# Kernel optimization log

Measured on AMD Instinct MI355X. Metric: run time of the kernel, lower is better.

## Reference

```python
import jax, jax.numpy as jnp
import numpy as np

B, S, H, K, HOP = 32, 512, 768, 4, 3


def setup_inputs() -> dict:
    key = jax.random.key(0)
    ks = jax.random.split(key, 18)
    sc = 0.02
    n = lambda k, shp: (jax.random.normal(k, shp, dtype=jnp.float32) * sc)
    inp = {
        "question": jax.random.normal(ks[0], (B, H), dtype=jnp.float32),
        "text": jax.random.normal(ks[1], (B, S, H), dtype=jnp.float32),
        # per-head MultiheadAttention params (stored as [in,out], i.e. W.T of torch Linear)
        "pw_W": n(ks[2], (K, H, H)), "pw_b": n(ks[3], (K, H)),
        "Ws_W": n(ks[4], (K, H, H)), "Ws_b": n(ks[5], (K, H)),
        "Wt_W": n(ks[6], (K, H, H)), "Wt_b": n(ks[7], (K, H)),
        "We_W": n(ks[8], (K, H)), "We_b": n(ks[9], (K,)),
        # head_weight: Linear(K -> 1)
        "headw_W": n(ks[10], (K,)), "headw_b": n(ks[11], (1,)),
        # GRUCell(input=2H, hidden=H); stored as [in, 3H] (r,z,n order as torch)
        "gru_Wih": n(ks[12], (2 * H, 3 * H)), "gru_Whh": n(ks[13], (H, 3 * H)),
        "gru_bih": n(ks[14], (3 * H,)), "gru_bhh": n(ks[15], (3 * H,)),
        "is_training": 0,
    }
    return inp


def _gru_cell(x, h, Wih, Whh, bih, bhh):
    gx = x @ Wih + bih            # [B,3H]
    gh = h @ Whh + bhh            # [B,3H]
    xr, xz, xn = jnp.split(gx, 3, axis=-1)
    hr, hz, hn = jnp.split(gh, 3, axis=-1)
    r = jax.nn.sigmoid(xr + hr)
    z = jax.nn.sigmoid(xz + hz)
    n = jnp.tanh(xn + r * hn)
    return (1.0 - z) * n + z * h


def reference(question, text, pw_W, pw_b, Ws_W, Ws_b, Wt_W, Wt_b, We_W, We_b,
              headw_W, headw_b, gru_Wih, gru_Whh, gru_bih, gru_bhh, is_training):
    # Dropout layers act as identity (eval mode).
    batch_idx = jnp.arange(text.shape[0])
    # text projection + W_s(text) are question-independent -> hoist out of hop loop
    text_p = jnp.einsum('bsh,khj->kbsj', text, pw_W) + pw_b[:, None, None, :]   # [K,B,S,H]
    W_hs = jnp.einsum('kbsh,khj->kbsj', text_p, Ws_W) + Ws_b[:, None, None, :]  # [K,B,S,H]

    h = jnp.zeros((text.shape[0], H), dtype=question.dtype)
    h_states = []
    predict_prob = None
    for hop in range(HOP):
        W_ht = jnp.einsum('bh,khj->kbj', question, Wt_W) + Wt_b[:, None, :]     # [K,B,H]
        scores = jnp.einsum('kbsh,kh->kbs', jnp.tanh(W_hs + W_ht[:, :, None, :]), We_W) \
                 + We_b[:, None, None]                                          # [K,B,S]
        alpha = jax.nn.softmax(scores, axis=2)                                  # softmax over S
        alpha_linear = jnp.einsum('kbs,k->bs', alpha, headw_W) + headw_b        # [B,S]
        scale = jnp.sqrt(jnp.sum(alpha_linear ** 2, axis=1, keepdims=True))
        prob = alpha_linear / scale
        if hop == 0:
            predict_prob = prob
        idx = jnp.argmax(alpha_linear, axis=1)                                  # [B]
        max_text = text[batch_idx, idx]                                         # [B,H]
        x = jnp.concatenate([question, max_text], axis=1)                       # [B,2H]
        h = _gru_cell(x, h, gru_Wih, gru_Whh, gru_bih, gru_bhh)
        h_states.append(h)
        question = h
    return predict_prob, jnp.stack(h_states, axis=1)                            # [B,S],[B,HOP,H]
```

## Files before the change

kernel.cpp:

```cpp
#include <hip/hip_runtime.h>

typedef unsigned short u16;
typedef __bf16 bf16x8 __attribute__((ext_vector_type(8)));
typedef float f32x4 __attribute__((ext_vector_type(4)));

#define NB 32
#define NS 512
#define NH 768
#define NK 4
#define NBS 16384
#define H3 2304
#define HH 589824

__device__ inline float bf2f(u16 u) {
    unsigned x = ((unsigned)u) << 16;
    return __builtin_bit_cast(float, x);
}
__device__ inline u16 f2bf(float f) {
    unsigned u = __builtin_bit_cast(unsigned, f);
    u += 0x7fffu + ((u >> 16) & 1u);
    return (u16)(u >> 16);
}
__device__ inline float tanh_fast(float x) {
    float e = __expf(2.f * x);
    return 1.f - 2.f * __builtin_amdgcn_rcpf(e + 1.f);
}
__device__ inline float sig_fast(float x) {
    return __builtin_amdgcn_rcpf(1.f + __expf(-x));
}
__device__ inline void gld16(const u16* g, u16* l) {
    __builtin_amdgcn_global_load_lds(
        (const __attribute__((address_space(1))) unsigned int*)g,
        (__attribute__((address_space(3))) unsigned int*)l, 16, 0, 0);
}


__global__ void prep_kernel(const float* __restrict__ WsW, const float* __restrict__ pwb,
                            const float* __restrict__ Wsb, float* __restrict__ combB,
                            const float* __restrict__ question,
                            float* __restrict__ q_f32, float* __restrict__ hT,
                            float* __restrict__ sx, float* __restrict__ sh,
                            const float* __restrict__ Web, float* __restrict__ scores,
                            const float* __restrict__ pwW,
                            u16* __restrict__ WsTH, u16* __restrict__ WsTL,
                            u16* __restrict__ pwH, u16* __restrict__ pwL,
                            const float* __restrict__ text, u16* __restrict__ textH,
                            int tier, int splitText)
{
    int bid = blockIdx.x, t = threadIdx.x;
    if (bid < 48) {
        int idx = bid * 64 + (t >> 2);
        int ph = t & 3;
        int k = idx / NH, j = idx % NH;
        const float* W = WsW + (long)k * HH + j;
        const float* pb = pwb + k * NH;
        float acc = 0.f;
        #pragma unroll 8
        for (int m = ph * 192; m < ph * 192 + 192; ++m)
            acc += pb[m] * W[(long)m * NH];
        acc += __shfl_xor(acc, 1);
        acc += __shfl_xor(acc, 2);
        if (ph == 0) combB[idx] = acc + Wsb[idx];
    } else if (bid < 144) {
        int idx = (bid - 48) * 256 + t;
        q_f32[idx] = question[idx];
    } else if (bid < 240) {
        int idx = (bid - 144) * 256 + t;
        hT[idx] = 0.f;
    } else if (bid < 816) {
        int idx = (bid - 240) * 256 + t;
        if (idx < 73728) sx[idx] = 0.f;
        else sh[idx - 73728] = 0.f;
    } else if (bid < 1072) {
        int idx = (bid - 816) * 256 + t;
        scores[idx] = Web[idx >> 14];
    } else if (bid < 3376) {
        if (tier < 2) return;
        __shared__ float tile[32][33];
        int bid2 = bid - 1072;
        int k = bid2 / 576, rem = bid2 % 576, tr = rem / 24, tc = rem % 24;
        const float* src = WsW + (long)k * HH;
        long dbase = (long)k * HH;
        int tx = t & 31, ty = t >> 5;
        #pragma unroll
        for (int i = 0; i < 4; ++i)
            tile[tx][ty + i*8] = src[(long)(tr*32 + ty + i*8) * NH + tc*32 + tx];
        __syncthreads();
        #pragma unroll
        for (int i = 0; i < 4; ++i) {
            float v = tile[ty + i*8][tx];
            u16 hv = f2bf(v);
            u16 lv = f2bf(v - bf2f(hv));
            long o = dbase + (long)(tc*32 + ty + i*8) * NH + tr*32 + tx;
            WsTH[o] = hv; WsTL[o] = lv;
        }
    } else if (bid < 5680) {
        if (tier < 2) return;
        long base = (long)(bid - 3376) * 1024 + t * 4;
        float4 v = *(const float4*)(pwW + base);
        ushort4 hv, lv;
        hv.x = f2bf(v.x); lv.x = f2bf(v.x - bf2f(hv.x));
        hv.y = f2bf(v.y); lv.y = f2bf(v.y - bf2f(hv.y));
        hv.z = f2bf(v.z); lv.z = f2bf(v.z - bf2f(hv.z));
        hv.w = f2bf(v.w); lv.w = f2bf(v.w - bf2f(hv.w));
        *(ushort4*)(pwH + base) = hv;
        *(ushort4*)(pwL + base) = lv;
    } else {
        if (!splitText) return;
        long base = (long)(bid - 5680) * 1024 + t * 4;
        float4 v = *(const float4*)(text + base);
        ushort4 hv;
        hv.x = f2bf(v.x);
        hv.y = f2bf(v.y);
        hv.z = f2bf(v.z);
        hv.w = f2bf(v.w);
        *(ushort4*)(textH + base) = hv;
    }
}

__global__ __launch_bounds__(256) void comb_mfma_kernel(
    const u16* __restrict__ WsTH, const u16* __restrict__ WsTL,
    const u16* __restrict__ pwH, const u16* __restrict__ pwL,
    u16* __restrict__ combTH, u16* __restrict__ combTL)
{
    __shared__ __align__(16) u16 AsH[128 * 32];
    __shared__ __align__(16) u16 AsL[128 * 32];
    __shared__ __align__(16) u16 BsH[128 * 32];
    __shared__ __align__(16) u16 BsL[128 * 32];
    const int t = threadIdx.x;
    const int wave = t >> 6, lane = t & 63;
    const int k = blockIdx.z;
    const long m0 = (long)blockIdx.x * 128;
    const int n0 = blockIdx.y * 128;
    const u16* AH = WsTH + (long)k * HH;
    const u16* AL = WsTL + (long)k * HH;
    const u16* BH = pwH + (long)k * HH;
    const u16* BL = pwL + (long)k * HH;

    const int r = t >> 2, ch = t & 3;
    const int wm = (wave & 1) * 64, wn = (wave >> 1) * 64;
    const int fr = lane & 15, fq = lane >> 4;

    f32x4 acc[4][4];
    #pragma unroll
    for (int i = 0; i < 4; ++i)
        #pragma unroll
        for (int j = 0; j < 4; ++j) acc[i][j] = (f32x4){0.f, 0.f, 0.f, 0.f};

    for (int k0 = 0; k0 < NH; k0 += 32) {
        gld16(AH + (m0 + r)      * NH + k0 + ch*8, AsH + t*8);
        gld16(AH + (m0 + 64 + r) * NH + k0 + ch*8, AsH + 2048 + t*8);
        gld16(AL + (m0 + r)      * NH + k0 + ch*8, AsL + t*8);
        gld16(AL + (m0 + 64 + r) * NH + k0 + ch*8, AsL + 2048 + t*8);
        gld16(BH + (long)(n0 + r)      * NH + k0 + ch*8, BsH + t*8);
        gld16(BH + (long)(n0 + 64 + r) * NH + k0 + ch*8, BsH + 2048 + t*8);
        gld16(BL + (long)(n0 + r)      * NH + k0 + ch*8, BsL + t*8);
        gld16(BL + (long)(n0 + 64 + r) * NH + k0 + ch*8, BsL + 2048 + t*8);
        __syncthreads();
        bf16x8 afH[4], afL[4], bfH[4], bfL[4];
        #pragma unroll
        for (int i = 0; i < 4; ++i) {
            afH[i] = *(const bf16x8*)(AsH + (wm + i*16 + fr)*32 + fq*8);
            afL[i] = *(const bf16x8*)(AsL + (wm + i*16 + fr)*32 + fq*8);
            bfH[i] = *(const bf16x8*)(BsH + (wn + i*16 + fr)*32 + fq*8);
            bfL[i] = *(const bf16x8*)(BsL + (wn + i*16 + fr)*32 + fq*8);
        }
        #pragma unroll
        for (int i = 0; i < 4; ++i)
            #pragma unroll
            for (int j = 0; j < 4; ++j) {
                acc[i][j] = __builtin_amdgcn_mfma_f32_16x16x32_bf16(afH[i], bfH[j], acc[i][j], 0, 0, 0);
                acc[i][j] = __builtin_amdgcn_mfma_f32_16x16x32_bf16(afH[i], bfL[j], acc[i][j], 0, 0, 0);
                acc[i][j] = __builtin_amdgcn_mfma_f32_16x16x32_bf16(afL[i], bfH[j], acc[i][j], 0, 0, 0);
            }
        __syncthreads();
    }
    long kb = (long)k * HH;
    #pragma unroll
    for (int i = 0; i < 4; ++i) {
        long m = m0 + wm + i*16 + fq*4;
        #pragma unroll
        for (int j = 0; j < 4; ++j) {
            long n = n0 + wn + j*16 + fr;
            #pragma unroll
            for (int rr = 0; rr < 4; ++rr) {
                float v = acc[i][j][rr];
                u16 hv = f2bf(v);
                u16 lv = f2bf(v - bf2f(hv));
                combTH[kb + (m + rr) * NH + n] = hv;
                combTL[kb + (m + rr) * NH + n] = lv;
            }
        }
    }
}

__global__ __launch_bounds__(256) void comb_valu_kernel(
    const float* __restrict__ pwW, const float* __restrict__ WsW,
    float* __restrict__ comb)
{
    __shared__ float AtT[32][68];
    __shared__ float Bt[32][132];
    const int t = threadIdx.x;
    const int m0 = blockIdx.x * 64, j0 = blockIdx.y * 128, k = blockIdx.z;
    const float* A = pwW + (long)k * HH;
    const float* B = WsW + (long)k * HH;
    const int r4 = (t >> 4) * 4, c8 = (t & 15) * 8;
    float acc[4][8];
    #pragma unroll
    for (int rr = 0; rr < 4; ++rr)
        #pragma unroll
        for (int cc = 0; cc < 8; ++cc) acc[rr][cc] = 0.f;
    for (int h0 = 0; h0 < NH; h0 += 32) {
        #pragma unroll
        for (int p = 0; p < 8; ++p) {
            int idx = p * 256 + t;
            int r = idx >> 5, hh = idx & 31;
            AtT[hh][r] = A[(long)(m0 + r) * NH + h0 + hh];
        }
        #pragma unroll
        for (int p = 0; p < 16; ++p) {
            int idx = p * 256 + t;
            int hh = idx >> 7, c = idx & 127;
            Bt[hh][c] = B[(long)(h0 + hh) * NH + j0 + c];
        }
        __syncthreads();
        for (int hh = 0; hh < 32; ++hh) {
            float4 av  = *(const float4*)&AtT[hh][r4];
            float4 bv0 = *(const float4*)&Bt[hh][c8];
            float4 bv1 = *(const float4*)&Bt[hh][c8 + 4];
            float a[4] = {av.x, av.y, av.z, av.w};
            float bb[8] = {bv0.x, bv0.y, bv0.z, bv0.w, bv1.x, bv1.y, bv1.z, bv1.w};
            #pragma unroll
            for (int rr = 0; rr < 4; ++rr)
                #pragma unroll
                for (int cc = 0; cc < 8; ++cc) acc[rr][cc] += a[rr] * bb[cc];
        }
        __syncthreads();
    }
    float* C = comb + (long)k * HH;
    #pragma unroll
    for (int rr = 0; rr < 4; ++rr)
        #pragma unroll
        for (int cc = 0; cc < 8; ++cc)
            C[(long)(m0 + r4 + rr) * NH + j0 + c8 + cc] = acc[rr][cc];
}

__global__ void split_combT_kernel(const float* __restrict__ comb,
                                   u16* __restrict__ combTH, u16* __restrict__ combTL)
{
    __shared__ float tile[32][33];
    int bid = blockIdx.x, t = threadIdx.x;
    int k = bid / 576, rem = bid % 576, tr = rem / 24, tc = rem % 24;
    const float* src = comb + (long)k * HH;
    long dbase = (long)k * HH;
    int tx = t & 31, ty = t >> 5;
    #pragma unroll
    for (int i = 0; i < 4; ++i)
        tile[tx][ty + i*8] = src[(long)(tr*32 + ty + i*8) * NH + tc*32 + tx];
    __syncthreads();
    #pragma unroll
    for (int i = 0; i < 4; ++i) {
        float v = tile[ty + i*8][tx];
        u16 hv = f2bf(v);
        u16 lv = f2bf(v - bf2f(hv));
        long o = dbase + (long)(tc*32 + ty + i*8) * NH + tr*32 + tx;
        combTH[o] = hv; combTL[o] = lv;
    }
}

template <int AM>
__global__ __launch_bounds__(256) void tp_gemm_kernel(
    const float* __restrict__ textf, const u16* __restrict__ textH,
    const u16* __restrict__ combTH, const u16* __restrict__ combTL,
    const float* __restrict__ W_ht, const float* __restrict__ WeW,
    u16* __restrict__ TP, float* __restrict__ scores)
{
    __shared__ __align__(16) u16 AsH[128 * 32];
    __shared__ __align__(16) u16 BsH[128 * 32];
    __shared__ __align__(16) u16 BsL[128 * 32];
    __shared__ float wht_s[128];
    __shared__ float we_s[128];
    __shared__ float sred[128];
    const int t = threadIdx.x;
    const int wave = t >> 6, lane = t & 63;
    const int k = blockIdx.z;
    const long m0 = (long)blockIdx.x * 128;
    const int n0 = blockIdx.y * 128;
    const int b = (int)(m0 >> 9), srow = (int)(m0 & 511);
    const u16* BH = combTH + (long)k * HH;
    const u16* BL = combTL + (long)k * HH;

    if (t < 128) {
        wht_s[t] = W_ht[((k << 5) + b) * NH + n0 + t];
        we_s[t]  = WeW[k * NH + n0 + t];
        sred[t]  = 0.f;
    }

    const int r = t >> 2, ch = t & 3;
    const int wm = (wave & 1) * 64, wn = (wave >> 1) * 64;
    const int fr = lane & 15, fq = lane >> 4;

    f32x4 acc[4][4];
    #pragma unroll
    for (int i = 0; i < 4; ++i)
        #pragma unroll
        for (int j = 0; j < 4; ++j) acc[i][j] = (f32x4){0.f, 0.f, 0.f, 0.f};

    for (int h0 = 0; h0 < NH; h0 += 32) {
        if (AM) {
            gld16(textH + (m0 + r)      * NH + h0 + ch*8, AsH + t*8);
            gld16(textH + (m0 + 64 + r) * NH + h0 + ch*8, AsH + 2048 + t*8);
        } else {
            #pragma unroll
            for (int p = 0; p < 4; ++p) {
                int task = p * 256 + t;
                int row = task >> 3, g = task & 7;
                float4 v = *(const float4*)(textf + (m0 + row) * NH + h0 + g*4);
                ushort4 hv;
                hv.x = f2bf(v.x);
                hv.y = f2bf(v.y);
                hv.z = f2bf(v.z);
                hv.w = f2bf(v.w);
                *(ushort4*)(AsH + row * 32 + g*4) = hv;
            }
        }
        gld16(BH + (long)(n0 + r)      * NH + h0 + ch*8, BsH + t*8);
        gld16(BH + (long)(n0 + 64 + r) * NH + h0 + ch*8, BsH + 2048 + t*8);
        gld16(BL + (long)(n0 + r)      * NH + h0 + ch*8, BsL + t*8);
        gld16(BL + (long)(n0 + 64 + r) * NH + h0 + ch*8, BsL + 2048 + t*8);
        __syncthreads();
        bf16x8 afH[4], bfH[4], bfL[4];
        #pragma unroll
        for (int i = 0; i < 4; ++i) {
            afH[i] = *(const bf16x8*)(AsH + (wm + i*16 + fr)*32 + fq*8);
            bfH[i] = *(const bf16x8*)(BsH + (wn + i*16 + fr)*32 + fq*8);
            bfL[i] = *(const bf16x8*)(BsL + (wn + i*16 + fr)*32 + fq*8);
        }
        #pragma unroll
        for (int i = 0; i < 4; ++i)
            #pragma unroll
            for (int j = 0; j < 4; ++j) {
                acc[i][j] = __builtin_amdgcn_mfma_f32_16x16x32_bf16(afH[i], bfH[j], acc[i][j], 0, 0, 0);
                acc[i][j] = __builtin_amdgcn_mfma_f32_16x16x32_bf16(afH[i], bfL[j], acc[i][j], 0, 0, 0);
            }
        __syncthreads();
    }
    u16* out = TP + ((long)k * NBS + m0) * NH + n0;
    #pragma unroll
    for (int i = 0; i < 4; ++i) {
        #pragma unroll
        for (int rr = 0; rr < 4; ++rr) {
            int m = wm + i*16 + fq*4 + rr;
            #pragma unroll
            for (int j = 0; j < 4; ++j) {
                int n = wn + j*16 + fr;
                out[(long)m * NH + n] = f2bf(acc[i][j][rr]);
            }
        }
    }
    #pragma unroll
    for (int i = 0; i < 4; ++i) {
        #pragma unroll
        for (int rr = 0; rr < 4; ++rr) {
            int m = wm + i*16 + fq*4 + rr;
            float part = 0.f;
            #pragma unroll
            for (int j = 0; j < 4; ++j) {
                int n = wn + j*16 + fr;
                part += tanh_fast(acc[i][j][rr] + wht_s[n]) * we_s[n];
            }
            part += __shfl_xor(part, 1);
            part += __shfl_xor(part, 2);
            part += __shfl_xor(part, 4);
            part += __shfl_xor(part, 8);
            if (fr == 0) atomicAdd(&sred[m], part);
        }
    }
    __syncthreads();
    if (t < 128)
        atomicAdd(&scores[(((k << 5) + b) << 9) + srow + t], sred[t]);
}

__global__ __launch_bounds__(256) void score_pass_kernel(
    const u16* __restrict__ TP, const float* __restrict__ W_ht,
    const float* __restrict__ WeW, const float* __restrict__ Web,
    float* __restrict__ scores)
{
    __shared__ __align__(16) float bias_s[NH];
    __shared__ __align__(16) float we_s[NH];
    const int t = threadIdx.x;
    const int k = blockIdx.z, b = blockIdx.y;
    const int s0 = blockIdx.x * 32;
    for (int i = t; i < NH; i += 256) {
        bias_s[i] = W_ht[((k << 5) + b) * NH + i];
        we_s[i]   = WeW[k * NH + i];
    }
    __syncthreads();
    const int wave = t >> 6, lane = t & 63;
    const u16* tpb = TP + ((long)k * NBS + (b << 9) + s0) * NH;
    const float web = Web[k];
    for (int sr = wave; sr < 32; sr += 4) {
        const u16* row = tpb + (long)sr * NH;
        float part = 0.f;
        #pragma unroll
        for (int p = 0; p < 3; ++p) {
            const int j = p * 256 + lane * 4;
            ushort4 v = *(const ushort4*)(row + j);
            float4 bb = *(const float4*)(bias_s + j);
            float4 ww = *(const float4*)(we_s + j);
            part += tanh_fast(bf2f(v.x) + bb.x) * ww.x;
            part += tanh_fast(bf2f(v.y) + bb.y) * ww.y;
            part += tanh_fast(bf2f(v.z) + bb.z) * ww.z;
            part += tanh_fast(bf2f(v.w) + bb.w) * ww.w;
        }
        part += __shfl_xor(part, 1);
        part += __shfl_xor(part, 2);
        part += __shfl_xor(part, 4);
        part += __shfl_xor(part, 8);
        part += __shfl_xor(part, 16);
        part += __shfl_xor(part, 32);
        if (lane == 0) scores[(((k << 5) + b) << 9) + s0 + sr] = part + web;
    }
}

__global__ void init_scores_kernel(const float* __restrict__ Web,
                                   float* __restrict__ scores, int koff)
{
    int idx = (koff << 14) + blockIdx.x * 256 + threadIdx.x;
    scores[idx] = Web[idx >> 14];
}

__global__ __launch_bounds__(256) void wht2_kernel(
    const float* __restrict__ q, const float* __restrict__ WtW,
    const float* __restrict__ combB, const float* __restrict__ Wtb,
    float* __restrict__ W_ht)
{
    int bid = blockIdx.x;
    int k = bid / 96, rem = bid % 96, b = rem / 3, jt = rem % 3;
    int j = jt * 256 + threadIdx.x;
    const float* W = WtW + (long)k * HH + j;
    const float* qb = q + b * NH;
    float acc = 0.f;
    #pragma unroll 8
    for (int h = 0; h < NH; ++h) acc += qb[h] * W[(long)h * NH];
    W_ht[(k*NB + b) * NH + j] = acc + Wtb[k * NH + j] + combB[k * NH + j];
}

template <int AM>
__global__ __launch_bounds__(256) void fused_scores_mfma(
    const float* __restrict__ textf,
    const u16* __restrict__ textH, const u16* __restrict__ textL,
    const u16* __restrict__ combTH, const u16* __restrict__ combTL,
    const float* __restrict__ W_ht,
    const float* __restrict__ WeW, float* __restrict__ scores, int koff)
{
    __shared__ __align__(16) u16 AsH[128 * 32];
    __shared__ __align__(16) u16 AsL[128 * 32];
    __shared__ __align__(16) u16 BsH[128 * 32];
    __shared__ __align__(16) u16 BsL[128 * 32];
    __shared__ float wht_s[128];
    __shared__ float we_s[128];
    __shared__ float sred[128];
    const int t = threadIdx.x;
    const int wave = t >> 6, lane = t & 63;
    const int k = koff + blockIdx.z;
    const long m0 = (long)blockIdx.x * 128;
    const int n0 = blockIdx.y * 128;
    const int b = (int)(m0 >> 9), srow = (int)(m0 & 511);
    const u16* BH = combTH + (long)k * HH;
    const u16* BL = combTL + (long)k * HH;

    if (t < 128) {
        wht_s[t] = W_ht[((k << 5) + b) * NH + n0 + t];
        we_s[t]  = WeW[k * NH + n0 + t];
        sred[t]  = 0.f;
    }

    const int r = t >> 2, ch = t & 3;
    const int wm = (wave & 1) * 64, wn = (wave >> 1) * 64;
    const int fr = lane & 15, fq = lane >> 4;

    f32x4 acc[4][4];
    #pragma unroll
    for (int i = 0; i < 4; ++i)
        #pragma unroll
        for (int j = 0; j < 4; ++j) acc[i][j] = (f32x4){0.f, 0.f, 0.f, 0.f};

    for (int h0 = 0; h0 < NH; h0 += 32) {
        if (AM) {
            gld16(textH + (m0 + r)      * NH + h0 + ch*8, AsH + t*8);
            gld16(textH + (m0 + 64 + r) * NH + h0 + ch*8, AsH + 2048 + t*8);
            gld16(textL + (m0 + r)      * NH + h0 + ch*8, AsL + t*8);
            gld16(textL + (m0 + 64 + r) * NH + h0 + ch*8, AsL + 2048 + t*8);
        } else {
            #pragma unroll
            for (int p = 0; p < 4; ++p) {
                int task = p * 256 + t;
                int row = task >> 3, g = task & 7;
                float4 v = *(const float4*)(textf + (m0 + row) * NH + h0 + g*4);
                ushort4 hv, lv;
                hv.x = f2bf(v.x); lv.x = f2bf(v.x - bf2f(hv.x));
                hv.y = f2bf(v.y); lv.y = f2bf(v.y - bf2f(hv.y));
                hv.z = f2bf(v.z); lv.z = f2bf(v.z - bf2f(hv.z));
                hv.w = f2bf(v.w); lv.w = f2bf(v.w - bf2f(hv.w));
                *(ushort4*)(AsH + row * 32 + g*4) = hv;
                *(ushort4*)(AsL + row * 32 + g*4) = lv;
            }
        }
        gld16(BH + (long)(n0 + r)      * NH + h0 + ch*8, BsH + t*8);
        gld16(BH + (long)(n0 + 64 + r) * NH + h0 + ch*8, BsH + 2048 + t*8);
        gld16(BL + (long)(n0 + r)      * NH + h0 + ch*8, BsL + t*8);
        gld16(BL + (long)(n0 + 64 + r) * NH + h0 + ch*8, BsL + 2048 + t*8);
        __syncthreads();
        bf16x8 afH[4], afL[4], bfH[4], bfL[4];
        #pragma unroll
        for (int i = 0; i < 4; ++i) {
            afH[i] = *(const bf16x8*)(AsH + (wm + i*16 + fr)*32 + fq*8);
            afL[i] = *(const bf16x8*)(AsL + (wm + i*16 + fr)*32 + fq*8);
            bfH[i] = *(const bf16x8*)(BsH + (wn + i*16 + fr)*32 + fq*8);
            bfL[i] = *(const bf16x8*)(BsL + (wn + i*16 + fr)*32 + fq*8);
        }
        #pragma unroll
        for (int i = 0; i < 4; ++i)
            #pragma unroll
            for (int j = 0; j < 4; ++j) {
                acc[i][j] = __builtin_amdgcn_mfma_f32_16x16x32_bf16(afH[i], bfH[j], acc[i][j], 0, 0, 0);
                acc[i][j] = __builtin_amdgcn_mfma_f32_16x16x32_bf16(afH[i], bfL[j], acc[i][j], 0, 0, 0);
                acc[i][j] = __builtin_amdgcn_mfma_f32_16x16x32_bf16(afL[i], bfH[j], acc[i][j], 0, 0, 0);
            }
        __syncthreads();
    }
    #pragma unroll
    for (int i = 0; i < 4; ++i) {
        #pragma unroll
        for (int rr = 0; rr < 4; ++rr) {
            int m = wm + i*16 + fq*4 + rr;
            float part = 0.f;
            #pragma unroll
            for (int j = 0; j < 4; ++j) {
                int n = wn + j*16 + fr;
                part += tanh_fast(acc[i][j][rr] + wht_s[n]) * we_s[n];
            }
            part += __shfl_xor(part, 1);
            part += __shfl_xor(part, 2);
            part += __shfl_xor(part, 4);
            part += __shfl_xor(part, 8);
            if (fr == 0) atomicAdd(&sred[m], part);
        }
    }
    __syncthreads();
    if (t < 128)
        atomicAdd(&scores[(((k << 5) + b) << 9) + srow + t], sred[t]);
}

__global__ __launch_bounds__(256) void fused_scores_valu(
    const float* __restrict__ text, const float* __restrict__ comb,
    const float* __restrict__ W_ht,
    const float* __restrict__ WeW, float* __restrict__ scores)
{
    __shared__ float AtT[32][68];
    __shared__ float Bt[32][132];
    __shared__ float wht_s[128];
    __shared__ float we_s[128];
    __shared__ float sred[64];
    const int t = threadIdx.x;
    const int row0 = blockIdx.x * 64;
    const int j0 = blockIdx.y * 128, k = blockIdx.z;
    const int b = row0 >> 9, s0 = row0 & 511;
    const float* B = comb + (long)k * HH;
    const int r4 = (t >> 4) * 4, c8 = (t & 15) * 8;
    if (t < 128) {
        wht_s[t] = W_ht[((k << 5) + b) * NH + j0 + t];
        we_s[t]  = WeW[k * NH + j0 + t];
    }
    if (t < 64) sred[t] = 0.f;
    float acc[4][8];
    #pragma unroll
    for (int rr = 0; rr < 4; ++rr)
        #pragma unroll
        for (int cc = 0; cc < 8; ++cc) acc[rr][cc] = 0.f;
    for (int h0 = 0; h0 < NH; h0 += 32) {
        #pragma unroll
        for (int p = 0; p < 8; ++p) {
            int idx = p * 256 + t;
            int r = idx >> 5, hh = idx & 31;
            AtT[hh][r] = text[(long)(row0 + r) * NH + h0 + hh];
        }
        #pragma unroll
        for (int p = 0; p < 16; ++p) {
            int idx = p * 256 + t;
            int hh = idx >> 7, c = idx & 127;
            Bt[hh][c] = B[(long)(h0 + hh) * NH + j0 + c];
        }
        __syncthreads();
        for (int hh = 0; hh < 32; ++hh) {
            float4 av  = *(const float4*)&AtT[hh][r4];
            float4 bv0 = *(const float4*)&Bt[hh][c8];
            float4 bv1 = *(const float4*)&Bt[hh][c8 + 4];
            float a[4] = {av.x, av.y, av.z, av.w};
            float bb[8] = {bv0.x, bv0.y, bv0.z, bv0.w, bv1.x, bv1.y, bv1.z, bv1.w};
            #pragma unroll
            for (int rr = 0; rr < 4; ++rr)
                #pragma unroll
                for (int cc = 0; cc < 8; ++cc) acc[rr][cc] += a[rr] * bb[cc];
        }
        __syncthreads();
    }
    float part[4] = {0.f, 0.f, 0.f, 0.f};
    #pragma unroll
    for (int rr = 0; rr < 4; ++rr)
        #pragma unroll
        for (int cc = 0; cc < 8; ++cc)
            part[rr] += tanh_fast(acc[rr][cc] + wht_s[c8 + cc]) * we_s[c8 + cc];
    #pragma unroll
    for (int rr = 0; rr < 4; ++rr)
        atomicAdd(&sred[r4 + rr], part[rr]);
    __syncthreads();
    if (t < 64)
        atomicAdd(&scores[(((k << 5) + b) << 9) + s0 + t], sred[t]);
}

__global__ void softmax_kernel(const float* __restrict__ scores,
                               const float* __restrict__ headw_W, const float* __restrict__ headw_b,
                               const float* __restrict__ text,
                               const float* __restrict__ q_f32,
                               float* __restrict__ xT, float* __restrict__ out_prob, int hop)
{
    __shared__ float sc[NK][NS];
    __shared__ float cred[4];
    __shared__ float cval[4];
    __shared__ int   cidx[4];
    int b = blockIdx.x, t = threadIdx.x;
    int wave = t >> 6, lane = t & 63;
    for (int i = t; i < NK * NS; i += 256) {
        int k = i >> 9, s = i & 511;
        sc[k][s] = scores[((k*NB + b) << 9) + s];
    }
    __syncthreads();
    float fac[NK];
    for (int k = 0; k < NK; ++k) {
        float v0 = sc[k][t], v1 = sc[k][t + 256];
        float m = fmaxf(v0, v1);
        #pragma unroll
        for (int o = 32; o > 0; o >>= 1) m = fmaxf(m, __shfl_xor(m, o));
        if (lane == 0) cred[wave] = m;
        __syncthreads();
        float mx = fmaxf(fmaxf(cred[0], cred[1]), fmaxf(cred[2], cred[3]));
        __syncthreads();
        float e0 = __expf(v0 - mx), e1 = __expf(v1 - mx);
        sc[k][t] = e0; sc[k][t + 256] = e1;
        float sm = e0 + e1;
        #pragma unroll
        for (int o = 32; o > 0; o >>= 1) sm += __shfl_xor(sm, o);
        if (lane == 0) cred[wave] = sm;
        __syncthreads();
        fac[k] = headw_W[k] / (cred[0] + cred[1] + cred[2] + cred[3]);
        __syncthreads();
    }
    float hwb = headw_b[0];
    float a0 = hwb, a1 = hwb;
    for (int k = 0; k < NK; ++k) { a0 += sc[k][t] * fac[k]; a1 += sc[k][t + 256] * fac[k]; }
    float ss = a0*a0 + a1*a1;
    #pragma unroll
    for (int o = 32; o > 0; o >>= 1) ss += __shfl_xor(ss, o);
    float bv; int bi;
    if (a0 >= a1) { bv = a0; bi = t; } else { bv = a1; bi = t + 256; }
    #pragma unroll
    for (int o = 1; o < 64; o <<= 1) {
        float ov = __shfl_xor(bv, o);
        int   oi = __shfl_xor(bi, o);
        if (ov > bv || (ov == bv && oi < bi)) { bv = ov; bi = oi; }
    }
    if (lane == 0) { cred[wave] = ss; cval[wave] = bv; cidx[wave] = bi; }
    __syncthreads();
    float scale = sqrtf(cred[0] + cred[1] + cred[2] + cred[3]);
    float mbv = cval[0]; int mbi = cidx[0];
    #pragma unroll
    for (int w = 1; w < 4; ++w)
        if (cval[w] > mbv || (cval[w] == mbv && cidx[w] < mbi)) { mbv = cval[w]; mbi = cidx[w]; }
    int idx = mbi;
    if (hop == 0) {
        out_prob[(b << 9) + t]       = a0 / scale;
        out_prob[(b << 9) + t + 256] = a1 / scale;
    }
    const float* trow = text + (long)(b * NS + idx) * NH;
    for (int i = t; i < NH; i += 256) {
        xT[i * NB + b]        = q_f32[b*NH + i];
        xT[(NH + i) * NB + b] = trow[i];
    }
}

__global__ __launch_bounds__(256) void gru_mm3_kernel(
    const float* __restrict__ Wih, const float* __restrict__ Whh,
    const float* __restrict__ xT, const float* __restrict__ hT,
    float* __restrict__ sx, float* __restrict__ sh)
{
    __shared__ float xs[8192];
    int t = threadIdx.x;
    int tj = t & 63, tq = t >> 6;
    int j = blockIdx.x * 64 + tj;
    int cg = blockIdx.y;
    const float* W; const float* src; float* dst; int c;
    if (cg < 6) { W = Wih; src = xT; dst = sx; c = cg; }
    else        { W = Whh; src = hT; dst = sh; c = cg - 6; }
    for (int idx = t; idx < 8192; idx += 256) xs[idx] = src[c * 8192 + idx];
    __syncthreads();
    float acc[8];
    #pragma unroll
    for (int bq = 0; bq < 8; ++bq) acc[bq] = 0.f;
    #pragma unroll 8
    for (int ii = 0; ii < 256; ++ii) {
        float w = W[(long)(c * 256 + ii) * H3 + j];
        #pragma unroll
        for (int bq = 0; bq < 8; ++bq) acc[bq] += xs[ii * 32 + tq * 8 + bq] * w;
    }
    #pragma unroll
    for (int bq = 0; bq < 8; ++bq)
        atomicAdd(&dst[(long)(tq * 8 + bq) * H3 + j], acc[bq]);
}

__global__ void gate_kernel(const float* __restrict__ bih, const float* __restrict__ bhh,
                            float* __restrict__ sx, float* __restrict__ sh,
                            float* __restrict__ hT, float* __restrict__ q_f32,
                            float* __restrict__ out_h, int hop)
{
    int gid = blockIdx.x * 256 + threadIdx.x;
    int b = gid / NH, j = gid % NH;
    float xr = bih[j]        + sx[b*H3 + j];
    float xz = bih[NH + j]   + sx[b*H3 + NH + j];
    float xn = bih[1536 + j] + sx[b*H3 + 1536 + j];
    float hr = bhh[j]        + sh[b*H3 + j];
    float hz = bhh[NH + j]   + sh[b*H3 + NH + j];
    float hn = bhh[1536 + j] + sh[b*H3 + 1536 + j];
    sx[b*H3 + j] = 0.f; sx[b*H3 + NH + j] = 0.f; sx[b*H3 + 1536 + j] = 0.f;
    sh[b*H3 + j] = 0.f; sh[b*H3 + NH + j] = 0.f; sh[b*H3 + 1536 + j] = 0.f;
    float r = sig_fast(xr + hr);
    float z = sig_fast(xz + hz);
    float n = tanh_fast(xn + r * hn);
    float hp = hT[j * NB + b];
    float hnew = (1.f - z) * n + z * hp;
    hT[j * NB + b] = hnew;
    q_f32[gid] = hnew;
    out_h[(long)(b * 3 + hop) * NH + j] = hnew;
}

extern "C" void kernel_launch(void* const* d_in, const int* in_sizes, int n_in,
                              void* d_out, int out_size, void* d_ws, size_t ws_size,
                              hipStream_t stream)
{
    const float* question = (const float*)d_in[0];
    const float* text     = (const float*)d_in[1];
    const float* pw_W     = (const float*)d_in[2];
    const float* pw_b     = (const float*)d_in[3];
    const float* Ws_W     = (const float*)d_in[4];
    const float* Ws_b     = (const float*)d_in[5];
    const float* Wt_W     = (const float*)d_in[6];
    const float* Wt_b     = (const float*)d_in[7];
    const float* We_W     = (const float*)d_in[8];
    const float* We_b     = (const float*)d_in[9];
    const float* headw_W  = (const float*)d_in[10];
    const float* headw_b  = (const float*)d_in[11];
    const float* Wih      = (const float*)d_in[12];
    const float* Whh      = (const float*)d_in[13];
    const float* bih      = (const float*)d_in[14];
    const float* bhh      = (const float*)d_in[15];

    char* ws = (char*)d_ws;
    float* comb   = (float*)(ws + 0);
    float* combB  = (float*)(ws + 9437184);
    float* W_ht   = (float*)(ws + 9449472);
    float* scores = (float*)(ws + 9842688);
    float* q_f32  = (float*)(ws + 10104832);
    float* hT     = (float*)(ws + 10203136);
    float* xT     = (float*)(ws + 10301440);
    float* sx     = (float*)(ws + 10498048);
    float* sh     = (float*)(ws + 10792960);
    u16*   combTH = (u16*)  (ws + 11087872);
    u16*   combTL = (u16*)  (ws + 15806464);
    u16*   TP     = (u16*)  (ws + 20525056);
    u16*   textH  = (u16*)  (ws + 121188352);
    u16*   WsTH   = (u16*)  (ws + 20525056);
    u16*   WsTL   = (u16*)  (ws + 25243648);
    u16*   pwH    = (u16*)  (ws + 29962240);
    u16*   pwL    = (u16*)  (ws + 34680832);

    int nstore = 0;
    if (ws_size >= (size_t)70856704) {
        long avail = (long)ws_size - 20525056L;
        nstore = (int)(avail / 25165824L);
        if (nstore > NK) nstore = NK;
    }
    const int tier = (nstore >= 1) ? 3
                   : (ws_size >= (size_t)20525056) ? 1 : 0;
    const bool haveTextH = (tier == 3) && (nstore == NK)
                        && (ws_size >= (size_t)146354176);

    float* out_prob = (float*)d_out;
    float* out_h    = (float*)d_out + NB * NS;

    const int prepGrid = haveTextH ? 17968 : (tier >= 2 ? 5680 : 1072);
    prep_kernel<<<prepGrid, 256, 0, stream>>>(
        Ws_W, pw_b, Ws_b, combB, question, q_f32, hT, sx, sh, We_b, scores,
        pw_W, WsTH, WsTL, pwH, pwL, text, textH,
        tier >= 3 ? 2 : tier, haveTextH ? 1 : 0);

    if (tier == 3) {
        comb_mfma_kernel<<<dim3(6, 6, 4), 256, 0, stream>>>(WsTH, WsTL, pwH, pwL,
                                                            combTH, combTL);
        wht2_kernel<<<384, 256, 0, stream>>>(q_f32, Wt_W, combB, Wt_b, W_ht);
        if (haveTextH) {
            tp_gemm_kernel<1><<<dim3(128, 6, nstore), 256, 0, stream>>>(
                text, textH, combTH, combTL, W_ht, We_W, TP, scores);
        } else {
            tp_gemm_kernel<0><<<dim3(128, 6, nstore), 256, 0, stream>>>(
                text, nullptr, combTH, combTL, W_ht, We_W, TP, scores);
        }
    } else {
        comb_valu_kernel<<<dim3(12, 6, 4), 256, 0, stream>>>(pw_W, Ws_W, comb);
        if (tier == 1)
            split_combT_kernel<<<2304, 256, 0, stream>>>(comb, combTH, combTL);
    }

    for (int hop = 0; hop < 3; ++hop) {
        if (tier == 3) {
            if (hop > 0) {
                wht2_kernel<<<384, 256, 0, stream>>>(q_f32, Wt_W, combB, Wt_b, W_ht);
                score_pass_kernel<<<dim3(16, 32, nstore), 256, 0, stream>>>(
                    TP, W_ht, We_W, We_b, scores);
                if (nstore < NK) {
                    init_scores_kernel<<<(NK - nstore) * 64, 256, 0, stream>>>(
                        We_b, scores, nstore);
                    fused_scores_mfma<0><<<dim3(128, 6, NK - nstore), 256, 0, stream>>>(
                        text, nullptr, nullptr, combTH, combTL, W_ht, We_W,
                        scores, nstore);
                }
            } else if (nstore < NK) {
                fused_scores_mfma<0><<<dim3(128, 6, NK - nstore), 256, 0, stream>>>(
                    text, nullptr, nullptr, combTH, combTL, W_ht, We_W,
                    scores, nstore);
            }
        } else {
            wht2_kernel<<<384, 256, 0, stream>>>(q_f32, Wt_W, combB, Wt_b, W_ht);
            init_scores_kernel<<<256, 256, 0, stream>>>(We_b, scores, 0);
            if (tier == 1)
                fused_scores_mfma<0><<<dim3(128, 6, 4), 256, 0, stream>>>(
                    text, nullptr, nullptr, combTH, combTL, W_ht, We_W, scores, 0);
            else
                fused_scores_valu<<<dim3(256, 6, 4), 256, 0, stream>>>(
                    text, comb, W_ht, We_W, scores);
        }
        softmax_kernel<<<32, 256, 0, stream>>>(scores, headw_W, headw_b, text,
                                               q_f32, xT, out_prob, hop);
        gru_mm3_kernel<<<dim3(36, 9), 256, 0, stream>>>(Wih, Whh, xT, hT, sx, sh);
        gate_kernel<<<96, 256, 0, stream>>>(bih, bhh, sx, sh, hT, q_f32, out_h, hop);
    }
}
```

Before: 632.9 us.

## Unfuse hop-0 score epilogue from TP GEMM and widen its K-tile to 64

The hop-0 tanh/We score reduction is removed from the text-projection GEMM epilogue. Hop 0 now uses the same wht2 plus score_pass path as later hops, reading the stored bf16 TP. The GEMM's K step doubles from 32 to 64, with larger shared-memory tiles and two MFMA sub-steps per barrier pair, which halves the number of sync iterations. In exchange it adds an extra read of TP for hop 0, uses more LDS per block, and the hop-0 scores now come from bf16-rounded TP instead of fp32 accumulators.

```diff
diff --git a/kernel.cpp b/kernel.cpp
--- a/kernel.cpp
+++ b/kernel.cpp
@@ -272,31 +272,20 @@
 __global__ __launch_bounds__(256) void tp_gemm_kernel(
     const float* __restrict__ textf, const u16* __restrict__ textH,
     const u16* __restrict__ combTH, const u16* __restrict__ combTL,
-    const float* __restrict__ W_ht, const float* __restrict__ WeW,
-    u16* __restrict__ TP, float* __restrict__ scores)
-{
-    __shared__ __align__(16) u16 AsH[128 * 32];
-    __shared__ __align__(16) u16 BsH[128 * 32];
-    __shared__ __align__(16) u16 BsL[128 * 32];
-    __shared__ float wht_s[128];
-    __shared__ float we_s[128];
-    __shared__ float sred[128];
+    u16* __restrict__ TP)
+{
+    __shared__ __align__(16) u16 AsH[128 * 64];
+    __shared__ __align__(16) u16 BsH[128 * 64];
+    __shared__ __align__(16) u16 BsL[128 * 64];
     const int t = threadIdx.x;
     const int wave = t >> 6, lane = t & 63;
     const int k = blockIdx.z;
     const long m0 = (long)blockIdx.x * 128;
     const int n0 = blockIdx.y * 128;
-    const int b = (int)(m0 >> 9), srow = (int)(m0 & 511);
     const u16* BH = combTH + (long)k * HH;
     const u16* BL = combTL + (long)k * HH;
 
-    if (t < 128) {
-        wht_s[t] = W_ht[((k << 5) + b) * NH + n0 + t];
-        we_s[t]  = WeW[k * NH + n0 + t];
-        sred[t]  = 0.f;
-    }
-
-    const int r = t >> 2, ch = t & 3;
+    const int r = t >> 3, ch = t & 7;
     const int wm = (wave & 1) * 64, wn = (wave >> 1) * 64;
     const int fr = lane & 15, fq = lane >> 4;
 
@@ -306,43 +295,48 @@
         #pragma unroll
         for (int j = 0; j < 4; ++j) acc[i][j] = (f32x4){0.f, 0.f, 0.f, 0.f};
 
-    for (int h0 = 0; h0 < NH; h0 += 32) {
+    for (int h0 = 0; h0 < NH; h0 += 64) {
         if (AM) {
-            gld16(textH + (m0 + r)      * NH + h0 + ch*8, AsH + t*8);
-            gld16(textH + (m0 + 64 + r) * NH + h0 + ch*8, AsH + 2048 + t*8);
+            #pragma unroll
+            for (int q = 0; q < 4; ++q)
+                gld16(textH + (m0 + q*32 + r) * NH + h0 + ch*8, AsH + q*2048 + t*8);
         } else {
             #pragma unroll
-            for (int p = 0; p < 4; ++p) {
+            for (int p = 0; p < 8; ++p) {
                 int task = p * 256 + t;
-                int row = task >> 3, g = task & 7;
+                int row = task >> 4, g = task & 15;
                 float4 v = *(const float4*)(textf + (m0 + row) * NH + h0 + g*4);
                 ushort4 hv;
                 hv.x = f2bf(v.x);
                 hv.y = f2bf(v.y);
                 hv.z = f2bf(v.z);
                 hv.w = f2bf(v.w);
-                *(ushort4*)(AsH + row * 32 + g*4) = hv;
+                *(ushort4*)(AsH + row * 64 + g*4) = hv;
             }
         }
-        gld16(BH + (long)(n0 + r)      * NH + h0 + ch*8, BsH + t*8);
-        gld16(BH + (long)(n0 + 64 + r) * NH + h0 + ch*8, BsH + 2048 + t*8);
-        gld16(BL + (long)(n0 + r)      * NH + h0 + ch*8, BsL + t*8);
-        gld16(BL + (long)(n0 + 64 + r) * NH + h0 + ch*8, BsL + 2048 + t*8);
-        __syncthreads();
-        bf16x8 afH[4], bfH[4], bfL[4];
-        #pragma unroll
-        for (int i = 0; i < 4; ++i) {
-            afH[i] = *(const bf16x8*)(AsH + (wm + i*16 + fr)*32 + fq*8);
-            bfH[i] = *(const bf16x8*)(BsH + (wn + i*16 + fr)*32 + fq*8);
-            bfL[i] = *(const bf16x8*)(BsL + (wn + i*16 + fr)*32 + fq*8);
-        }
-        #pragma unroll
-        for (int i = 0; i < 4; ++i)
-            #pragma unroll
-            for (int j = 0; j < 4; ++j) {
-                acc[i][j] = __builtin_amdgcn_mfma_f32_16x16x32_bf16(afH[i], bfH[j], acc[i][j], 0, 0, 0);
-                acc[i][j] = __builtin_amdgcn_mfma_f32_16x16x32_bf16(afH[i], bfL[j], acc[i][j], 0, 0, 0);
+        #pragma unroll
+        for (int q = 0; q < 4; ++q) {
+            gld16(BH + (long)(n0 + q*32 + r) * NH + h0 + ch*8, BsH + q*2048 + t*8);
+            gld16(BL + (long)(n0 + q*32 + r) * NH + h0 + ch*8, BsL + q*2048 + t*8);
+        }
+        __syncthreads();
+        #pragma unroll
+        for (int ks = 0; ks < 2; ++ks) {
+            bf16x8 afH[4], bfH[4], bfL[4];
+            #pragma unroll
+            for (int i = 0; i < 4; ++i) {
+                afH[i] = *(const bf16x8*)(AsH + (wm + i*16 + fr)*64 + ks*32 + fq*8);
+                bfH[i] = *(const bf16x8*)(BsH + (wn + i*16 + fr)*64 + ks*32 + fq*8);
+                bfL[i] = *(const bf16x8*)(BsL + (wn + i*16 + fr)*64 + ks*32 + fq*8);
             }
+            #pragma unroll
+            for (int i = 0; i < 4; ++i)
+                #pragma unroll
+                for (int j = 0; j < 4; ++j) {
+                    acc[i][j] = __builtin_amdgcn_mfma_f32_16x16x32_bf16(afH[i], bfH[j], acc[i][j], 0, 0, 0);
+                    acc[i][j] = __builtin_amdgcn_mfma_f32_16x16x32_bf16(afH[i], bfL[j], acc[i][j], 0, 0, 0);
+                }
+        }
         __syncthreads();
     }
     u16* out = TP + ((long)k * NBS + m0) * NH + n0;
@@ -358,27 +352,6 @@
             }
         }
     }
-    #pragma unroll
-    for (int i = 0; i < 4; ++i) {
-        #pragma unroll
-        for (int rr = 0; rr < 4; ++rr) {
-            int m = wm + i*16 + fq*4 + rr;
-            float part = 0.f;
-            #pragma unroll
-            for (int j = 0; j < 4; ++j) {
-                int n = wn + j*16 + fr;
-                part += tanh_fast(acc[i][j][rr] + wht_s[n]) * we_s[n];
-            }
-            part += __shfl_xor(part, 1);
-            part += __shfl_xor(part, 2);
-            part += __shfl_xor(part, 4);
-            part += __shfl_xor(part, 8);
-            if (fr == 0) atomicAdd(&sred[m], part);
-        }
-    }
-    __syncthreads();
-    if (t < 128)
-        atomicAdd(&scores[(((k << 5) + b) << 9) + srow + t], sred[t]);
 }
 
 __global__ __launch_bounds__(256) void score_pass_kernel(
@@ -807,13 +780,12 @@
     if (tier == 3) {
         comb_mfma_kernel<<<dim3(6, 6, 4), 256, 0, stream>>>(WsTH, WsTL, pwH, pwL,
                                                             combTH, combTL);
-        wht2_kernel<<<384, 256, 0, stream>>>(q_f32, Wt_W, combB, Wt_b, W_ht);
         if (haveTextH) {
             tp_gemm_kernel<1><<<dim3(128, 6, nstore), 256, 0, stream>>>(
-                text, textH, combTH, combTL, W_ht, We_W, TP, scores);
+                text, textH, combTH, combTL, TP);
         } else {
             tp_gemm_kernel<0><<<dim3(128, 6, nstore), 256, 0, stream>>>(
-                text, nullptr, combTH, combTL, W_ht, We_W, TP, scores);
+                text, nullptr, combTH, combTL, TP);
         }
     } else {
         comb_valu_kernel<<<dim3(12, 6, 4), 256, 0, stream>>>(pw_W, Ws_W, comb);
@@ -822,32 +794,26 @@
     }
 
     for (int hop = 0; hop < 3; ++hop) {
+        wht2_kernel<<<384, 256, 0, stream>>>(q_f32, Wt_W, combB, Wt_b, W_ht);
         if (tier == 3) {
-            if (hop > 0) {
-                wht2_kernel<<<384, 256, 0, stream>>>(q_f32, Wt_W, combB, Wt_b, W_ht);
-                score_pass_kernel<<<dim3(16, 32, nstore), 256, 0, stream>>>(
-                    TP, W_ht, We_W, We_b, scores);
-                if (nstore < NK) {
+            score_pass_kernel<<<dim3(16, 32, nstore), 256, 0, stream>>>(
+                TP, W_ht, We_W, We_b, scores);
+            if (nstore < NK) {
+                if (hop > 0)
                     init_scores_kernel<<<(NK - nstore) * 64, 256, 0, stream>>>(
                         We_b, scores, nstore);
-                    fused_scores_mfma<0><<<dim3(128, 6, NK - nstore), 256, 0, stream>>>(
-                        text, nullptr, nullptr, combTH, combTL, W_ht, We_W,
-                        scores, nstore);
-                }
-            } else if (nstore < NK) {
                 fused_scores_mfma<0><<<dim3(128, 6, NK - nstore), 256, 0, stream>>>(
                     text, nullptr, nullptr, combTH, combTL, W_ht, We_W,
                     scores, nstore);
             }
+        } else if (tier == 1) {
+            init_scores_kernel<<<256, 256, 0, stream>>>(We_b, scores, 0);
+            fused_scores_mfma<0><<<dim3(128, 6, 4), 256, 0, stream>>>(
+                text, nullptr, nullptr, combTH, combTL, W_ht, We_W, scores, 0);
         } else {
-            wht2_kernel<<<384, 256, 0, stream>>>(q_f32, Wt_W, combB, Wt_b, W_ht);
             init_scores_kernel<<<256, 256, 0, stream>>>(We_b, scores, 0);
-            if (tier == 1)
-                fused_scores_mfma<0><<<dim3(128, 6, 4), 256, 0, stream>>>(
-                    text, nullptr, nullptr, combTH, combTL, W_ht, We_W, scores, 0);
-            else
-                fused_scores_valu<<<dim3(256, 6, 4), 256, 0, stream>>>(
-                    text, comb, W_ht, We_W, scores);
+            fused_scores_valu<<<dim3(256, 6, 4), 256, 0, stream>>>(
+                text, comb, W_ht, We_W, scores);
         }
         softmax_kernel<<<32, 256, 0, stream>>>(scores, headw_W, headw_b, text,
                                                q_f32, xT, out_prob, hop);
```

Measured after the change: 630.7 us. Within noise of the previous version (-0.4%).
